# Kernel tuning notes

Hardware: AMD Instinct MI355X
Metric: run time of the kernel (lower is better)

Reference implementation:

```python
import jax, jax.numpy as jnp
import numpy as np

DIM, C_HID, N_HEADS = 128, 32, 4
INF = 1.0e9
LN_EPS = 1e-5


def setup_inputs() -> dict:
    key = jax.random.key(0)
    ks = jax.random.split(key, 10)
    B, I, J, C, H, D = 1, 256, 256, DIM, N_HEADS, C_HID
    s = 0.02
    return {
        "x": jax.random.normal(ks[0], (B, I, J, C), jnp.float32),
        "mask": jnp.ones((B, I, J), jnp.float32),
        "ln_w": jnp.ones((C,), jnp.float32),
        "ln_b": jnp.zeros((C,), jnp.float32),
        "tri_w": jax.random.normal(ks[1], (C, H), jnp.float32) * s,  # bias=False
        "q_w": jax.random.normal(ks[2], (C, H * D), jnp.float32) * s,
        "k_w": jax.random.normal(ks[3], (C, H * D), jnp.float32) * s,
        "v_w": jax.random.normal(ks[4], (C, H * D), jnp.float32) * s,
        "g_w": jax.random.normal(ks[5], (C, H * D), jnp.float32) * s,
        "g_b": jnp.ones((H * D,), jnp.float32),  # gating init: bias=1
        "o_w": jax.random.normal(ks[6], (H * D, C), jnp.float32) * s,
        "o_b": jnp.zeros((C,), jnp.float32),
    }


def _layer_norm(x, w, b):
    mu = jnp.mean(x, axis=-1, keepdims=True)
    var = jnp.mean(jnp.square(x - mu), axis=-1, keepdims=True)
    return (x - mu) * jax.lax.rsqrt(var + LN_EPS) * w + b


def reference(x, mask, ln_w, ln_b, tri_w, q_w, k_w, v_w, g_w, g_b, o_w, o_b):
    # starting=True: no transpose. x: [B, I, J, C], mask: [B, I, J]
    B, I, J, C = x.shape
    H, D = N_HEADS, C_HID
    xn = _layer_norm(x, ln_w, ln_b)

    # mask bias: [B, I, 1, 1, J]; triangle bias: [B, 1, H, I(J), J]
    mask_bias = (INF * (mask - 1.0))[:, :, None, None, :]
    tri_bias = jnp.einsum("bijc,ch->bhij", xn, tri_w)[:, None]

    def proj(w):  # [B, I, H, J, D]
        return (xn @ w).reshape(B, I, J, H, D).transpose(0, 1, 3, 2, 4)

    q = proj(q_w) * (D ** -0.5)
    k = proj(k_w)
    v = proj(v_w)

    logits = jnp.einsum("bihqd,bihkd->bihqk", q, k) + mask_bias + tri_bias
    a = jax.nn.softmax(logits, axis=-1)
    o = jnp.einsum("bihqk,bihkd->bihqd", a, v).transpose(0, 1, 3, 2, 4)  # [B,I,J,H,D]

    g = jax.nn.sigmoid(xn @ g_w + g_b).reshape(B, I, J, H, D)
    o = (o * g).reshape(B, I, J, H * D)
    return o @ o_w + o_b
```

## Files before the change

### kernel.cpp

```cpp
#include <hip/hip_runtime.h>
#include <hip/hip_bf16.h>
#include <math.h>

#define LOG2E_ 1.4426950408889634f

typedef short short8 __attribute__((ext_vector_type(8)));
typedef float f32x4 __attribute__((ext_vector_type(4)));
typedef int int4v __attribute__((ext_vector_type(4)));

#if defined(__has_builtin)
#if __has_builtin(__builtin_amdgcn_exp2f)
#define EXP2F(x) __builtin_amdgcn_exp2f(x)
#else
#define EXP2F(x) exp2f(x)
#endif
#else
#define EXP2F(x) exp2f(x)
#endif

static __device__ __forceinline__ unsigned short f2bf(float f) {
    union { float f; unsigned int u; } c; c.f = f;
    c.u += 0x7fffu + ((c.u >> 16) & 1u);
    return (unsigned short)(c.u >> 16);
}
static __device__ __forceinline__ int pk2bf(float a, float b) {
    union { __hip_bfloat162 h; int i; } u;
    u.h = __float22bfloat162_rn(make_float2(a, b));
    return u.i;
}
static __device__ __forceinline__ void load_lds16(const void* g, void* l) {
    __builtin_amdgcn_global_load_lds(
        (const __attribute__((address_space(1))) void*)g,
        (__attribute__((address_space(3))) void*)l, 16, 0, 0);
}

__global__ __launch_bounds__(256) void ln_prep_kernel(
    const float* __restrict__ x, const float* __restrict__ ln_w,
    const float* __restrict__ ln_b, const float* __restrict__ tri_w,
    const float* __restrict__ qw, const float* __restrict__ kw,
    const float* __restrict__ vw, const float* __restrict__ gw,
    const float* __restrict__ ow,
    unsigned short* __restrict__ xn, float* __restrict__ triT,
    char* __restrict__ wimg)
{
    const int bid = blockIdx.x, tid = threadIdx.x;
    if (bid >= 8192) {
        int id = (bid - 8192) * 256 + tid;
        int h = id / 2688;
        int b = (id - h * 2688) * 16;
        unsigned short v[8];
        if (b < 32768) {
            int sl = b >> 13;
            int bi = b & 8191;
            int row = bi >> 8;
            int c8 = ((bi >> 4) & 15) ^ (row & 7);
            const float* src = (sl == 0) ? qw : (sl == 1) ? kw : (sl == 2) ? vw : gw;
            float scale = (sl == 0) ? (0.17677669529663687f * LOG2E_) : 1.0f;
            int R = h * 32 + row;
            #pragma unroll
            for (int e = 0; e < 8; ++e)
                v[e] = f2bf(src[(c8 * 8 + e) * 128 + R] * scale);
        } else {
            int o = b - 32768;
            int n = o / 80;
            int k8 = (o - n * 80) >> 4;
            if (k8 < 4) {
                #pragma unroll
                for (int e = 0; e < 8; ++e)
                    v[e] = f2bf(ow[(h * 32 + k8 * 8 + e) * 128 + n]);
            } else {
                #pragma unroll
                for (int e = 0; e < 8; ++e) v[e] = 0;
            }
        }
        *(short8*)(wimg + h * 43008 + b) = *(short8*)v;
        return;
    }

    const int row = bid * 8 + (tid >> 5);
    const int l = tid & 31;

    float4 xv = *(const float4*)(x + (size_t)row * 128 + l * 4);
    float s = (xv.x + xv.y) + (xv.z + xv.w);
    #pragma unroll
    for (int mk = 16; mk >= 1; mk >>= 1) s += __shfl_xor(s, mk, 64);
    float mu = s * (1.0f / 128.0f);

    float d0 = xv.x - mu, d1 = xv.y - mu, d2 = xv.z - mu, d3 = xv.w - mu;
    float sq = (d0 * d0 + d1 * d1) + (d2 * d2 + d3 * d3);
    #pragma unroll
    for (int mk = 16; mk >= 1; mk >>= 1) sq += __shfl_xor(sq, mk, 64);
    float rstd = rsqrtf(sq * (1.0f / 128.0f) + 1e-5f);

    float4 wv = *(const float4*)(ln_w + l * 4);
    float4 bv = *(const float4*)(ln_b + l * 4);
    float n0 = d0 * rstd * wv.x + bv.x;
    float n1 = d1 * rstd * wv.y + bv.y;
    float n2 = d2 * rstd * wv.z + bv.z;
    float n3 = d3 * rstd * wv.w + bv.w;

    ushort4 xo;
    xo.x = f2bf(n0); xo.y = f2bf(n1); xo.z = f2bf(n2); xo.w = f2bf(n3);
    *(ushort4*)(xn + (size_t)row * 128 + l * 4) = xo;

    float4 t0 = *(const float4*)(tri_w + (l * 4 + 0) * 4);
    float4 t1 = *(const float4*)(tri_w + (l * 4 + 1) * 4);
    float4 t2 = *(const float4*)(tri_w + (l * 4 + 2) * 4);
    float4 t3 = *(const float4*)(tri_w + (l * 4 + 3) * 4);
    float ax = (n0 * t0.x + n1 * t1.x) + (n2 * t2.x + n3 * t3.x);
    float ay = (n0 * t0.y + n1 * t1.y) + (n2 * t2.y + n3 * t3.y);
    float az = (n0 * t0.z + n1 * t1.z) + (n2 * t2.z + n3 * t3.z);
    float aw = (n0 * t0.w + n1 * t1.w) + (n2 * t2.w + n3 * t3.w);
    #pragma unroll
    for (int mk = 16; mk >= 1; mk >>= 1) {
        ax += __shfl_xor(ax, mk, 64);
        ay += __shfl_xor(ay, mk, 64);
        az += __shfl_xor(az, mk, 64);
        aw += __shfl_xor(aw, mk, 64);
    }
    if (l < 4) {
        float v = (l == 0) ? ax : (l == 1) ? ay : (l == 2) ? az : aw;
        int q = row >> 8, kc = row & 255;
        int off = l * 65536 + (q >> 4) * 4096 + (kc >> 4) * 256
                + (q & 15) * 16 + (kc & 15);
        triT[off] = v * LOG2E_;
    }
}

__global__ __launch_bounds__(1024, 4) void mega_kernel(
    const unsigned short* __restrict__ xn, const char* __restrict__ wimg,
    const float* __restrict__ g_b, const float* __restrict__ mask,
    const float* __restrict__ triT, const float* __restrict__ o_b,
    float* __restrict__ out)
{
    __shared__ __align__(16) char WBUF[2 * 43008];
    __shared__ __align__(16) unsigned short Qg[256 * 40];
    __shared__ __align__(16) unsigned short Kl[256 * 40];
    __shared__ __align__(16) unsigned short Vc[32 * 264];
    __shared__ float mb[256];

    const int i = blockIdx.x;
    const int tid = threadIdx.x;
    const int w = tid >> 6, lane = tid & 63, g = lane >> 4, m = lane & 15;
    const f32x4 zero = {0.f, 0.f, 0.f, 0.f};

    short8 xa[4];
    #pragma unroll
    for (int kc = 0; kc < 4; ++kc)
        xa[kc] = *(const short8*)(xn + (size_t)(i * 256 + w * 16 + m) * 128
                                  + kc * 32 + 8 * g);
    if (tid < 256) mb[tid] = (mask[i * 256 + tid] - 1.0f) * (1.0e9f * LOG2E_);

    {
        const char* src = wimg + w * 1024 + lane * 16;
        char* dst = WBUF + w * 1024;
        load_lds16(src, dst);
        load_lds16(src + 16384, dst + 16384);
        if (w < 10) load_lds16(src + 32768, dst + 32768);
    }
    __syncthreads();

    const int srcA = ((g & 1) << 1) | (g >> 1);
    const int idxA = (srcA * 16 + m) * 4;
    const int idxB = idxA ^ 64;
    const bool low = (lane < 32);
    const bool odd = (g & 1);
    const char* VcB0 = (const char*)Vc + m * 528;
    const char* VcB1 = (const char*)Vc + (16 + m) * 528;

    f32x4 oacc[8];
    #pragma unroll
    for (int nt = 0; nt < 8; ++nt) oacc[nt] = zero;

    const int qrow = w * 16 + m;

    #pragma unroll 1
    for (int h = 0; h < 4; ++h) {
        const char* wb = WBUF + (h & 1) * 43008;

        {
            f32x4 aq[2] = {zero, zero}, ak[2] = {zero, zero};
            #pragma unroll
            for (int kc = 0; kc < 4; ++kc) {
                short8 b0[2], b1[2];
                #pragma unroll
                for (int nt = 0; nt < 2; ++nt) {
                    int row = nt * 16 + m;
                    int off = (row * 256 + kc * 64 + 16 * g) ^ ((row & 7) << 4);
                    b0[nt] = *(const short8*)(wb + off);
                    b1[nt] = *(const short8*)(wb + 8192 + off);
                }
                #pragma unroll
                for (int nt = 0; nt < 2; ++nt) {
                    aq[nt] = __builtin_amdgcn_mfma_f32_16x16x32_bf16(b0[nt], xa[kc], aq[nt], 0, 0, 0);
                    ak[nt] = __builtin_amdgcn_mfma_f32_16x16x32_bf16(b1[nt], xa[kc], ak[nt], 0, 0, 0);
                }
            }
            #pragma unroll
            for (int nt = 0; nt < 2; ++nt) {
                int col = nt * 16 + 4 * g;
                ushort4 q4, k4;
                q4.x = f2bf(aq[nt][0]); q4.y = f2bf(aq[nt][1]);
                q4.z = f2bf(aq[nt][2]); q4.w = f2bf(aq[nt][3]);
                k4.x = f2bf(ak[nt][0]); k4.y = f2bf(ak[nt][1]);
                k4.z = f2bf(ak[nt][2]); k4.w = f2bf(ak[nt][3]);
                *(ushort4*)(Qg + qrow * 40 + col) = q4;
                *(ushort4*)(Kl + qrow * 40 + col) = k4;
            }
        }

        f32x4 gacc[2];
        {
            f32x4 av4[2] = {zero, zero}, ag[2] = {zero, zero};
            #pragma unroll
            for (int kc = 0; kc < 4; ++kc) {
                short8 b0[2], b1[2];
                #pragma unroll
                for (int nt = 0; nt < 2; ++nt) {
                    int row = nt * 16 + m;
                    int off = (row * 256 + kc * 64 + 16 * g) ^ ((row & 7) << 4);
                    b0[nt] = *(const short8*)(wb + 16384 + off);
                    b1[nt] = *(const short8*)(wb + 24576 + off);
                }
                #pragma unroll
                for (int nt = 0; nt < 2; ++nt) {
                    av4[nt] = __builtin_amdgcn_mfma_f32_16x16x32_bf16(xa[kc], b0[nt], av4[nt], 0, 0, 0);
                    ag[nt]  = __builtin_amdgcn_mfma_f32_16x16x32_bf16(b1[nt], xa[kc], ag[nt], 0, 0, 0);
                }
            }
            #pragma unroll
            for (int nt = 0; nt < 2; ++nt) {
                ushort4 v4;
                v4.x = f2bf(av4[nt][0]); v4.y = f2bf(av4[nt][1]);
                v4.z = f2bf(av4[nt][2]); v4.w = f2bf(av4[nt][3]);
                *(ushort4*)(Vc + (nt * 16 + m) * 264 + w * 16 + 4 * g) = v4;
                int col = nt * 16 + 4 * g;
                #pragma unroll
                for (int r = 0; r < 4; ++r)
                    gacc[nt][r] = 1.0f / (1.0f + __expf(-(ag[nt][r] + g_b[h * 32 + col + r])));
            }
        }
        __syncthreads();

        if (h < 3) {
            const char* src = wimg + (h + 1) * 43008 + w * 1024 + lane * 16;
            char* dst = WBUF + ((h + 1) & 1) * 43008 + w * 1024;
            load_lds16(src, dst);
            load_lds16(src + 16384, dst + 16384);
            if (w < 10) load_lds16(src + 32768, dst + 32768);
        }

        const short8 qf = *(const short8*)((const char*)Qg + qrow * 80 + 16 * g);
        const float* triQ = triT + h * 65536 + w * 4096 + m * 16 + 4 * g;

        float ls = 0.f;
        f32x4 o0 = zero, o1 = zero;

        #pragma unroll
        for (int c = 0; c < 8; ++c) {
            int d00, d01, d10, d11;
            {
                const int kt = 2 * c;
                short8 af = *(const short8*)((const char*)Kl + (kt * 16 + m) * 80 + 16 * g);
                f32x4 bias = *(const f32x4*)(mb + kt * 16 + 4 * g)
                           + *(const f32x4*)(triQ + kt * 256);
                f32x4 acc = __builtin_amdgcn_mfma_f32_16x16x32_bf16(af, qf, bias, 0, 0, 0);
                float p0 = EXP2F(acc[0]);
                float p1 = EXP2F(acc[1]);
                float p2 = EXP2F(acc[2]);
                float p3 = EXP2F(acc[3]);
                ls += (p0 + p1) + (p2 + p3);
                d00 = pk2bf(p0, p1); d01 = pk2bf(p2, p3);
            }
            {
                const int kt = 2 * c + 1;
                short8 af = *(const short8*)((const char*)Kl + (kt * 16 + m) * 80 + 16 * g);
                f32x4 bias = *(const f32x4*)(mb + kt * 16 + 4 * g)
                           + *(const f32x4*)(triQ + kt * 256);
                f32x4 acc = __builtin_amdgcn_mfma_f32_16x16x32_bf16(af, qf, bias, 0, 0, 0);
                float p0 = EXP2F(acc[0]);
                float p1 = EXP2F(acc[1]);
                float p2 = EXP2F(acc[2]);
                float p3 = EXP2F(acc[3]);
                ls += (p0 + p1) + (p2 + p3);
                d10 = pk2bf(p0, p1); d11 = pk2bf(p2, p3);
            }
            int pk0 = odd ? d10 : d00;
            int pk1 = odd ? d11 : d01;
            int pk2 = odd ? d00 : d10;
            int pk3 = odd ? d01 : d11;

            int dA0 = __builtin_amdgcn_ds_bpermute(idxA, pk0);
            int dA1 = __builtin_amdgcn_ds_bpermute(idxA, pk1);
            int dB0 = __builtin_amdgcn_ds_bpermute(idxB, pk2);
            int dB1 = __builtin_amdgcn_ds_bpermute(idxB, pk3);
            int4v bi;
            bi.x = low ? dA0 : dB0;
            bi.y = low ? dA1 : dB1;
            bi.z = low ? dB0 : dA0;
            bi.w = low ? dB1 : dA1;
            short8 bs = __builtin_bit_cast(short8, bi);

            short8 av0 = *(const short8*)(VcB0 + c * 64 + 16 * g);
            short8 av1 = *(const short8*)(VcB1 + c * 64 + 16 * g);
            o0 = __builtin_amdgcn_mfma_f32_16x16x32_bf16(av0, bs, o0, 0, 0, 0);
            o1 = __builtin_amdgcn_mfma_f32_16x16x32_bf16(av1, bs, o1, 0, 0, 0);
        }
        ls += __shfl_xor(ls, 16, 64);
        ls += __shfl_xor(ls, 32, 64);
        float inv = 1.0f / ls;

        ushort4 s0, s1;
        s0.x = f2bf(o0[0] * inv * gacc[0][0]);
        s0.y = f2bf(o0[1] * inv * gacc[0][1]);
        s0.z = f2bf(o0[2] * inv * gacc[0][2]);
        s0.w = f2bf(o0[3] * inv * gacc[0][3]);
        s1.x = f2bf(o1[0] * inv * gacc[1][0]);
        s1.y = f2bf(o1[1] * inv * gacc[1][1]);
        s1.z = f2bf(o1[2] * inv * gacc[1][2]);
        s1.w = f2bf(o1[3] * inv * gacc[1][3]);
        *(ushort4*)(Qg + qrow * 40 + 4 * g) = s0;
        *(ushort4*)(Qg + qrow * 40 + 16 + 4 * g) = s1;

        {
            short8 a = *(const short8*)((const char*)Qg + qrow * 80 + 16 * g);
            #pragma unroll
            for (int nt = 0; nt < 8; ++nt) {
                short8 b = *(const short8*)(wb + 32768 + (nt * 16 + m) * 80 + 16 * g);
                oacc[nt] = __builtin_amdgcn_mfma_f32_16x16x32_bf16(b, a, oacc[nt], 0, 0, 0);
            }
        }
        __syncthreads();
    }

    const int orow = i * 256 + qrow;
    #pragma unroll
    for (int nt = 0; nt < 8; ++nt) {
        int col = nt * 16 + 4 * g;
        float4 bv = *(const float4*)(o_b + col);
        float4 o;
        o.x = oacc[nt][0] + bv.x;
        o.y = oacc[nt][1] + bv.y;
        o.z = oacc[nt][2] + bv.z;
        o.w = oacc[nt][3] + bv.w;
        *(float4*)(out + (size_t)orow * 128 + col) = o;
    }
}

extern "C" void kernel_launch(void* const* d_in, const int* in_sizes, int n_in,
                              void* d_out, int out_size, void* d_ws, size_t ws_size,
                              hipStream_t stream) {
    (void)in_sizes; (void)n_in; (void)out_size; (void)ws_size;
    const float* x    = (const float*)d_in[0];
    const float* mask = (const float*)d_in[1];
    const float* ln_w = (const float*)d_in[2];
    const float* ln_b = (const float*)d_in[3];
    const float* tri_w= (const float*)d_in[4];
    const float* q_w  = (const float*)d_in[5];
    const float* k_w  = (const float*)d_in[6];
    const float* v_w  = (const float*)d_in[7];
    const float* g_w  = (const float*)d_in[8];
    const float* g_b  = (const float*)d_in[9];
    const float* o_w  = (const float*)d_in[10];
    const float* o_b  = (const float*)d_in[11];

    char* ws = (char*)d_ws;
    unsigned short* xn  = (unsigned short*)(ws);
    float*          tri = (float*)(ws + 16777216);
    char*           wimg= (char*)(ws + 17825792);

    ln_prep_kernel<<<8234, 256, 0, stream>>>(x, ln_w, ln_b, tri_w,
                                             q_w, k_w, v_w, g_w, o_w,
                                             xn, tri, wimg);
    mega_kernel<<<256, 1024, 0, stream>>>(xn, wimg, g_b, mask, tri, o_b,
                                          (float*)d_out);
}
```

Before: 72.44 us.

## Precompute K/V for all heads upfront, read weights from global, drop per-head barriers

Weights are no longer staged into LDS with double-buffered async loads. Each wave reads them straight from global memory, relying on cache. K and V for all four heads are computed in one prologue and stored in LDS, so the head loop needs no __syncthreads, since Q and the gated output are per-wave rows. The LDS row stride is cut from 40 to 36 shorts. The cost is more global/L2 traffic for weight fragments, plus a larger LDS footprint for four heads of K and V, and the narrower stride may change bank conflicts.

```diff
diff --git a/kernel.cpp b/kernel.cpp
--- a/kernel.cpp
+++ b/kernel.cpp
@@ -27,11 +27,6 @@
     union { __hip_bfloat162 h; int i; } u;
     u.h = __float22bfloat162_rn(make_float2(a, b));
     return u.i;
-}
-static __device__ __forceinline__ void load_lds16(const void* g, void* l) {
-    __builtin_amdgcn_global_load_lds(
-        (const __attribute__((address_space(1))) void*)g,
-        (__attribute__((address_space(3))) void*)l, 16, 0, 0);
 }
 
 __global__ __launch_bounds__(256) void ln_prep_kernel(
@@ -133,30 +128,52 @@
     const float* __restrict__ triT, const float* __restrict__ o_b,
     float* __restrict__ out)
 {
-    __shared__ __align__(16) char WBUF[2 * 43008];
-    __shared__ __align__(16) unsigned short Qg[256 * 40];
-    __shared__ __align__(16) unsigned short Kl[256 * 40];
-    __shared__ __align__(16) unsigned short Vc[32 * 264];
+    __shared__ __align__(16) unsigned short Kl[4 * 256 * 36];
+    __shared__ __align__(16) unsigned short Vc[4 * 32 * 264];
+    __shared__ __align__(16) unsigned short Qg[256 * 36];
     __shared__ float mb[256];
 
     const int i = blockIdx.x;
     const int tid = threadIdx.x;
     const int w = tid >> 6, lane = tid & 63, g = lane >> 4, m = lane & 15;
     const f32x4 zero = {0.f, 0.f, 0.f, 0.f};
+    const int qrow = w * 16 + m;
 
     short8 xa[4];
     #pragma unroll
     for (int kc = 0; kc < 4; ++kc)
-        xa[kc] = *(const short8*)(xn + (size_t)(i * 256 + w * 16 + m) * 128
+        xa[kc] = *(const short8*)(xn + (size_t)(i * 256 + qrow) * 128
                                   + kc * 32 + 8 * g);
     if (tid < 256) mb[tid] = (mask[i * 256 + tid] - 1.0f) * (1.0e9f * LOG2E_);
 
-    {
-        const char* src = wimg + w * 1024 + lane * 16;
-        char* dst = WBUF + w * 1024;
-        load_lds16(src, dst);
-        load_lds16(src + 16384, dst + 16384);
-        if (w < 10) load_lds16(src + 32768, dst + 32768);
+    #pragma unroll 1
+    for (int h = 0; h < 4; ++h) {
+        const char* wK = wimg + h * 43008 + 8192;
+        const char* wV = wimg + h * 43008 + 16384;
+        f32x4 ak[2] = {zero, zero}, av4[2] = {zero, zero};
+        #pragma unroll
+        for (int kc = 0; kc < 4; ++kc) {
+            #pragma unroll
+            for (int nt = 0; nt < 2; ++nt) {
+                int row = nt * 16 + m;
+                int off = (row * 256 + kc * 64 + 16 * g) ^ ((row & 7) << 4);
+                short8 kf = *(const short8*)(wK + off);
+                short8 vf = *(const short8*)(wV + off);
+                ak[nt]  = __builtin_amdgcn_mfma_f32_16x16x32_bf16(kf, xa[kc], ak[nt], 0, 0, 0);
+                av4[nt] = __builtin_amdgcn_mfma_f32_16x16x32_bf16(xa[kc], vf, av4[nt], 0, 0, 0);
+            }
+        }
+        #pragma unroll
+        for (int nt = 0; nt < 2; ++nt) {
+            int col = nt * 16 + 4 * g;
+            ushort4 k4, v4;
+            k4.x = f2bf(ak[nt][0]); k4.y = f2bf(ak[nt][1]);
+            k4.z = f2bf(ak[nt][2]); k4.w = f2bf(ak[nt][3]);
+            v4.x = f2bf(av4[nt][0]); v4.y = f2bf(av4[nt][1]);
+            v4.z = f2bf(av4[nt][2]); v4.w = f2bf(av4[nt][3]);
+            *(ushort4*)(Kl + (h * 256 + qrow) * 36 + col) = k4;
+            *(ushort4*)(Vc + h * 8448 + (nt * 16 + m) * 264 + w * 16 + 4 * g) = v4;
+        }
     }
     __syncthreads();
 
@@ -165,92 +182,49 @@
     const int idxB = idxA ^ 64;
     const bool low = (lane < 32);
     const bool odd = (g & 1);
-    const char* VcB0 = (const char*)Vc + m * 528;
-    const char* VcB1 = (const char*)Vc + (16 + m) * 528;
 
     f32x4 oacc[8];
     #pragma unroll
     for (int nt = 0; nt < 8; ++nt) oacc[nt] = zero;
-
-    const int qrow = w * 16 + m;
 
     #pragma unroll 1
     for (int h = 0; h < 4; ++h) {
-        const char* wb = WBUF + (h & 1) * 43008;
-
+        const char* wQ = wimg + h * 43008;
+        const char* wG = wimg + h * 43008 + 24576;
+        const char* wO = wimg + h * 43008 + 32768;
+        const char* KlH = (const char*)Kl + h * 256 * 72;
+        const char* VcB0 = (const char*)Vc + h * 16896 + m * 528;
+        const char* VcB1 = VcB0 + 16 * 528;
+
+        f32x4 gacc[2];
         {
-            f32x4 aq[2] = {zero, zero}, ak[2] = {zero, zero};
+            f32x4 aq[2] = {zero, zero}, ag[2] = {zero, zero};
             #pragma unroll
             for (int kc = 0; kc < 4; ++kc) {
-                short8 b0[2], b1[2];
                 #pragma unroll
                 for (int nt = 0; nt < 2; ++nt) {
                     int row = nt * 16 + m;
                     int off = (row * 256 + kc * 64 + 16 * g) ^ ((row & 7) << 4);
-                    b0[nt] = *(const short8*)(wb + off);
-                    b1[nt] = *(const short8*)(wb + 8192 + off);
-                }
-                #pragma unroll
-                for (int nt = 0; nt < 2; ++nt) {
-                    aq[nt] = __builtin_amdgcn_mfma_f32_16x16x32_bf16(b0[nt], xa[kc], aq[nt], 0, 0, 0);
-                    ak[nt] = __builtin_amdgcn_mfma_f32_16x16x32_bf16(b1[nt], xa[kc], ak[nt], 0, 0, 0);
+                    short8 qfw = *(const short8*)(wQ + off);
+                    short8 gfw = *(const short8*)(wG + off);
+                    aq[nt] = __builtin_amdgcn_mfma_f32_16x16x32_bf16(qfw, xa[kc], aq[nt], 0, 0, 0);
+                    ag[nt] = __builtin_amdgcn_mfma_f32_16x16x32_bf16(gfw, xa[kc], ag[nt], 0, 0, 0);
                 }
             }
             #pragma unroll
             for (int nt = 0; nt < 2; ++nt) {
                 int col = nt * 16 + 4 * g;
-                ushort4 q4, k4;
+                ushort4 q4;
                 q4.x = f2bf(aq[nt][0]); q4.y = f2bf(aq[nt][1]);
                 q4.z = f2bf(aq[nt][2]); q4.w = f2bf(aq[nt][3]);
-                k4.x = f2bf(ak[nt][0]); k4.y = f2bf(ak[nt][1]);
-                k4.z = f2bf(ak[nt][2]); k4.w = f2bf(ak[nt][3]);
-                *(ushort4*)(Qg + qrow * 40 + col) = q4;
-                *(ushort4*)(Kl + qrow * 40 + col) = k4;
-            }
-        }
-
-        f32x4 gacc[2];
-        {
-            f32x4 av4[2] = {zero, zero}, ag[2] = {zero, zero};
-            #pragma unroll
-            for (int kc = 0; kc < 4; ++kc) {
-                short8 b0[2], b1[2];
-                #pragma unroll
-                for (int nt = 0; nt < 2; ++nt) {
-                    int row = nt * 16 + m;
-                    int off = (row * 256 + kc * 64 + 16 * g) ^ ((row & 7) << 4);
-                    b0[nt] = *(const short8*)(wb + 16384 + off);
-                    b1[nt] = *(const short8*)(wb + 24576 + off);
-                }
-                #pragma unroll
-                for (int nt = 0; nt < 2; ++nt) {
-                    av4[nt] = __builtin_amdgcn_mfma_f32_16x16x32_bf16(xa[kc], b0[nt], av4[nt], 0, 0, 0);
-                    ag[nt]  = __builtin_amdgcn_mfma_f32_16x16x32_bf16(b1[nt], xa[kc], ag[nt], 0, 0, 0);
-                }
-            }
-            #pragma unroll
-            for (int nt = 0; nt < 2; ++nt) {
-                ushort4 v4;
-                v4.x = f2bf(av4[nt][0]); v4.y = f2bf(av4[nt][1]);
-                v4.z = f2bf(av4[nt][2]); v4.w = f2bf(av4[nt][3]);
-                *(ushort4*)(Vc + (nt * 16 + m) * 264 + w * 16 + 4 * g) = v4;
-                int col = nt * 16 + 4 * g;
+                *(ushort4*)(Qg + qrow * 36 + col) = q4;
                 #pragma unroll
                 for (int r = 0; r < 4; ++r)
                     gacc[nt][r] = 1.0f / (1.0f + __expf(-(ag[nt][r] + g_b[h * 32 + col + r])));
             }
         }
-        __syncthreads();
-
-        if (h < 3) {
-            const char* src = wimg + (h + 1) * 43008 + w * 1024 + lane * 16;
-            char* dst = WBUF + ((h + 1) & 1) * 43008 + w * 1024;
-            load_lds16(src, dst);
-            load_lds16(src + 16384, dst + 16384);
-            if (w < 10) load_lds16(src + 32768, dst + 32768);
-        }
-
-        const short8 qf = *(const short8*)((const char*)Qg + qrow * 80 + 16 * g);
+
+        const short8 qf = *(const short8*)((const char*)Qg + qrow * 72 + 16 * g);
         const float* triQ = triT + h * 65536 + w * 4096 + m * 16 + 4 * g;
 
         float ls = 0.f;
@@ -261,7 +235,7 @@
             int d00, d01, d10, d11;
             {
                 const int kt = 2 * c;
-                short8 af = *(const short8*)((const char*)Kl + (kt * 16 + m) * 80 + 16 * g);
+                short8 af = *(const short8*)(KlH + (kt * 16 + m) * 72 + 16 * g);
                 f32x4 bias = *(const f32x4*)(mb + kt * 16 + 4 * g)
                            + *(const f32x4*)(triQ + kt * 256);
                 f32x4 acc = __builtin_amdgcn_mfma_f32_16x16x32_bf16(af, qf, bias, 0, 0, 0);
@@ -274,7 +248,7 @@
             }
             {
                 const int kt = 2 * c + 1;
-                short8 af = *(const short8*)((const char*)Kl + (kt * 16 + m) * 80 + 16 * g);
+                short8 af = *(const short8*)(KlH + (kt * 16 + m) * 72 + 16 * g);
                 f32x4 bias = *(const f32x4*)(mb + kt * 16 + 4 * g)
                            + *(const f32x4*)(triQ + kt * 256);
                 f32x4 acc = __builtin_amdgcn_mfma_f32_16x16x32_bf16(af, qf, bias, 0, 0, 0);
@@ -319,18 +293,17 @@
         s1.y = f2bf(o1[1] * inv * gacc[1][1]);
         s1.z = f2bf(o1[2] * inv * gacc[1][2]);
         s1.w = f2bf(o1[3] * inv * gacc[1][3]);
-        *(ushort4*)(Qg + qrow * 40 + 4 * g) = s0;
-        *(ushort4*)(Qg + qrow * 40 + 16 + 4 * g) = s1;
+        *(ushort4*)(Qg + qrow * 36 + 4 * g) = s0;
+        *(ushort4*)(Qg + qrow * 36 + 16 + 4 * g) = s1;
 
         {
-            short8 a = *(const short8*)((const char*)Qg + qrow * 80 + 16 * g);
+            short8 a = *(const short8*)((const char*)Qg + qrow * 72 + 16 * g);
             #pragma unroll
             for (int nt = 0; nt < 8; ++nt) {
-                short8 b = *(const short8*)(wb + 32768 + (nt * 16 + m) * 80 + 16 * g);
+                short8 b = *(const short8*)(wO + (nt * 16 + m) * 80 + 16 * g);
                 oacc[nt] = __builtin_amdgcn_mfma_f32_16x16x32_bf16(b, a, oacc[nt], 0, 0, 0);
             }
         }
-        __syncthreads();
     }
 
     const int orow = i * 256 + qrow;
```

After: 121.1 us. 67.1% more time.
